# Kernel optimization log

Hardware: AMD Instinct MI355X
Metric: run time of the kernel (lower is better)

The kernel has to match this reference:

```python
import jax, jax.numpy as jnp
import numpy as np

DIM = 512
HEADS = 8
DIM_HEAD = 64
INNER = HEADS * DIM_HEAD  # 512
EPS = 1e-5


def _per_head_layernorm(t, gamma, beta):
    # t: [b, h, n, k]; gamma/beta: [h, k] (distinct LayerNorm per head)
    mu = jnp.mean(t, axis=-1, keepdims=True)
    var = jnp.mean(jnp.square(t - mu), axis=-1, keepdims=True)
    t_hat = (t - mu) * jax.lax.rsqrt(var + EPS)
    return t_hat * gamma[None, :, None, :] + beta[None, :, None, :]


def setup_inputs() -> dict:
    key = jax.random.key(0)
    ks = jax.random.split(key, 6)
    x = jax.random.normal(ks[0], (4, 8192, DIM), dtype=jnp.float32)
    # xavier_normal_ with gain=1e-4 on to_qkv weight [3*inner, dim]
    std_qkv = 1e-4 * np.sqrt(2.0 / (3 * INNER + DIM))
    W_qkv = jax.random.normal(ks[1], (3 * INNER, DIM), dtype=jnp.float32) * std_qkv
    gamma_K = jnp.ones((HEADS, DIM_HEAD), dtype=jnp.float32)
    beta_K = jnp.zeros((HEADS, DIM_HEAD), dtype=jnp.float32)
    gamma_V = jnp.ones((HEADS, DIM_HEAD), dtype=jnp.float32)
    beta_V = jnp.zeros((HEADS, DIM_HEAD), dtype=jnp.float32)
    std_out = np.sqrt(1.0 / INNER)
    W_out = jax.random.uniform(ks[2], (DIM, INNER), dtype=jnp.float32, minval=-std_out, maxval=std_out)
    b_out = jax.random.uniform(ks[3], (DIM,), dtype=jnp.float32, minval=-std_out, maxval=std_out)
    return {"x": x, "W_qkv": W_qkv, "gamma_K": gamma_K, "beta_K": beta_K,
            "gamma_V": gamma_V, "beta_V": beta_V, "W_out": W_out, "b_out": b_out}


def reference(x, W_qkv, gamma_K, beta_K, gamma_V, beta_V, W_out, b_out):
    b, n, _ = x.shape
    qkv = jnp.einsum('bnd,ed->bne', x, W_qkv)  # [b, n, 3*inner]
    q, k, v = jnp.split(qkv, 3, axis=-1)

    def to_heads(t):  # [b, n, h*k] -> [b, h, n, k]
        return t.reshape(b, n, HEADS, DIM_HEAD).transpose(0, 2, 1, 3)

    q, k, v = to_heads(q), to_heads(k), to_heads(v)
    k = _per_head_layernorm(k, gamma_K, beta_K)
    v = _per_head_layernorm(v, gamma_V, beta_V)

    # Galerkin linear attention: (K^T V)/n then Q @ (.)  -> O(n * d^2)
    p_attn = jnp.einsum('bhnk,bhnv->bhkv', k, v) / n  # [b, h, k, k]
    out = jnp.einsum('bhnk,bhkv->bhnv', q, p_attn)    # [b, h, n, k]
    out = out.transpose(0, 2, 1, 3).reshape(b, n, INNER)
    return jnp.einsum('bne,de->bnd', out, W_out) + b_out
```

## Files before the change

kernel.cpp:

```cpp
#include <hip/hip_runtime.h>


typedef __attribute__((ext_vector_type(8))) short bf16x8;
typedef __attribute__((ext_vector_type(4))) float f32x4;
typedef __attribute__((ext_vector_type(4))) unsigned short u16x4;
typedef __attribute__((ext_vector_type(4))) unsigned int u32x4;

__device__ __forceinline__ unsigned short f2bf(float f) {
  unsigned int u = __builtin_bit_cast(unsigned int, f);
  u += 0x7FFFu + ((u >> 16) & 1u);
  return (unsigned short)(u >> 16);
}

__device__ __forceinline__ unsigned int cvt2(float lo, float hi) {
  return ((unsigned int)f2bf(hi) << 16) | (unsigned int)f2bf(lo);
}

__device__ __forceinline__ f32x4 mfma16(bf16x8 a, bf16x8 b, f32x4 c) {
  return __builtin_amdgcn_mfma_f32_16x16x32_bf16(a, b, c, 0, 0, 0);
}

__device__ __forceinline__ void gload16(const void* g, void* l) {
  __builtin_amdgcn_global_load_lds(
      (const __attribute__((address_space(1))) void*)g,
      (__attribute__((address_space(3))) void*)l, 16, 0, 0);
}

__global__ void k_cvt_w(const float* __restrict__ Wqkv,
                        const float* __restrict__ Wout,
                        unsigned short* __restrict__ Wb,
                        unsigned short* __restrict__ Wob) {
  int i = blockIdx.x * 256 + threadIdx.x;
  const float4* src;
  u16x4* dst;
  if (i < 196608) { src = (const float4*)Wqkv + i; dst = (u16x4*)Wb + i; }
  else { i -= 196608; src = (const float4*)Wout + i; dst = (u16x4*)Wob + i; }
  float4 v = *src;
  u16x4 o;
  o[0] = f2bf(v.x); o[1] = f2bf(v.y); o[2] = f2bf(v.z); o[3] = f2bf(v.w);
  *dst = o;
}

__launch_bounds__(256, 3)
__global__ void k1_kvp(const float* __restrict__ x,
                       const unsigned short* __restrict__ wqkvb,
                       const float* __restrict__ gK, const float* __restrict__ bK,
                       const float* __restrict__ gV, const float* __restrict__ bV,
                       float* __restrict__ Ppart) {
  __shared__ __align__(16) unsigned short As[8192];
  __shared__ __align__(16) unsigned short Bs[8192];
  const int bid = (int)blockIdx.x;
  const int wgid = (bid & 7) * 256 + (bid >> 3);
  const int rt = wgid >> 3, h = wgid & 7;
  const int tid = (int)threadIdx.x;
  const int l = tid & 63, w = tid >> 6;
  const int wr = w >> 1, wc = w & 1;
  const int g = l >> 4, c16 = l & 15;
  const int row0 = rt * 128;
  const int swz = ((l & 7) ^ (l >> 3)) * 8;

  const float* gx = x + (size_t)(row0 + w * 32 + (l >> 3)) * 512 + swz;
  const int bcol = (w < 2) ? (512 + h * 64 + w * 32) : (1024 + h * 64 + (w - 2) * 32);
  const unsigned short* gsB = wqkvb + (bcol + (l >> 3)) * 512 + swz;
  unsigned short* la = As + w * 2048 + l * 8;

  f32x4 acc[4][4] = {};
  float4 pf[8];

#pragma unroll
  for (int j = 0; j < 4; ++j) {
    pf[2 * j]     = *(const float4*)(gx + j * 4096);
    pf[2 * j + 1] = *(const float4*)(gx + j * 4096 + 4);
  }

  for (int kt = 0; kt < 8; ++kt) {
#pragma unroll
    for (int j = 0; j < 4; ++j) {
      u32x4 c;
      c[0] = cvt2(pf[2 * j].x, pf[2 * j].y);
      c[1] = cvt2(pf[2 * j].z, pf[2 * j].w);
      c[2] = cvt2(pf[2 * j + 1].x, pf[2 * j + 1].y);
      c[3] = cvt2(pf[2 * j + 1].z, pf[2 * j + 1].w);
      *(u32x4*)(la + j * 512) = c;
    }
#pragma unroll
    for (int j = 0; j < 4; ++j)
      gload16(gsB + kt * 64 + j * 8 * 512, Bs + w * 2048 + j * 512);
    __builtin_amdgcn_sched_barrier(0);
    if (kt < 7) {
#pragma unroll
      for (int j = 0; j < 4; ++j) {
        pf[2 * j]     = *(const float4*)(gx + (kt + 1) * 64 + j * 4096);
        pf[2 * j + 1] = *(const float4*)(gx + (kt + 1) * 64 + j * 4096 + 4);
      }
      asm volatile("s_waitcnt vmcnt(8) lgkmcnt(0)" ::: "memory");
    } else {
      asm volatile("s_waitcnt vmcnt(0) lgkmcnt(0)" ::: "memory");
    }
    __builtin_amdgcn_sched_barrier(0);
    __builtin_amdgcn_s_barrier();
#pragma unroll
    for (int ks = 0; ks < 2; ++ks) {
      const int kcol = (ks * 32 + g * 8) ^ ((c16 & 7) << 3);
      bf16x8 af[4], bfv[4];
#pragma unroll
      for (int mi = 0; mi < 4; ++mi)
        af[mi] = *(const bf16x8*)&As[(wr * 64 + mi * 16 + c16) * 64 + kcol];
#pragma unroll
      for (int ni = 0; ni < 4; ++ni)
        bfv[ni] = *(const bf16x8*)&Bs[(wc * 64 + ni * 16 + c16) * 64 + kcol];
#pragma unroll
      for (int mi = 0; mi < 4; ++mi)
#pragma unroll
        for (int ni = 0; ni < 4; ++ni)
          acc[mi][ni] = mfma16(af[mi], bfv[ni], acc[mi][ni]);
    }
    __builtin_amdgcn_sched_barrier(0);
    __builtin_amdgcn_s_barrier();
  }

  const float* gamma = (wc == 0) ? gK : gV;
  const float* beta  = (wc == 0) ? bK : bV;
  float gm[4], bt[4];
#pragma unroll
  for (int ni = 0; ni < 4; ++ni) {
    gm[ni] = gamma[h * 64 + ni * 16 + c16];
    bt[ni] = beta[h * 64 + ni * 16 + c16];
  }
  unsigned short* dst = (wc == 0) ? As : Bs;
#pragma unroll
  for (int mi = 0; mi < 4; ++mi) {
    float mean4[4], rs4[4];
#pragma unroll
    for (int r = 0; r < 4; ++r) {
      float a0 = acc[mi][0][r], a1 = acc[mi][1][r];
      float a2 = acc[mi][2][r], a3 = acc[mi][3][r];
      float s1 = a0 + a1 + a2 + a3;
      float s2 = a0 * a0 + a1 * a1 + a2 * a2 + a3 * a3;
#pragma unroll
      for (int m = 1; m <= 8; m <<= 1) {
        s1 += __shfl_xor(s1, m, 64);
        s2 += __shfl_xor(s2, m, 64);
      }
      const float mean = s1 * (1.0f / 64.0f);
      const float var = s2 * (1.0f / 64.0f) - mean * mean;
      mean4[r] = mean;
      rs4[r] = rsqrtf(var + 1e-5f);
    }
    const int n0 = wr * 64 + mi * 16 + g * 4;
#pragma unroll
    for (int ni = 0; ni < 4; ++ni) {
      u16x4 o;
#pragma unroll
      for (int r = 0; r < 4; ++r)
        o[r] = f2bf((acc[mi][ni][r] - mean4[r]) * rs4[r] * gm[ni] + bt[ni]);
      *(u16x4*)&dst[(ni * 16 + c16) * 128 + (((n0 >> 3) ^ c16) << 3) + (n0 & 7)] = o;
    }
  }
  __syncthreads();

  f32x4 pacc[4] = {};
#pragma unroll
  for (int ks = 0; ks < 4; ++ks) {
    const int grp = ((ks * 4 + g) ^ c16) << 3;
    bf16x8 af = *(const bf16x8*)&As[(w * 16 + c16) * 128 + grp];
#pragma unroll
    for (int ni = 0; ni < 4; ++ni) {
      bf16x8 bv = *(const bf16x8*)&Bs[(ni * 16 + c16) * 128 + grp];
      pacc[ni] = mfma16(af, bv, pacc[ni]);
    }
  }
  const int bh = (rt >> 6) * 8 + h;
  float* Pp = Ppart + ((size_t)(bh * 64 + (rt & 63))) * 4096;
#pragma unroll
  for (int ni = 0; ni < 4; ++ni)
#pragma unroll
    for (int r = 0; r < 4; ++r)
      Pp[(w * 16 + g * 4 + r) * 64 + ni * 16 + c16] = pacc[ni][r];
}

__launch_bounds__(256)
__global__ void k_preduce(const float* __restrict__ Ppart,
                          float* __restrict__ P) {
  const int bh = blockIdx.x;
  const int e = blockIdx.y * 256 + threadIdx.x;
  const float* src = Ppart + (size_t)bh * 64 * 4096 + e;
  float s = 0.f;
#pragma unroll 8
  for (int sl = 0; sl < 64; ++sl) s += src[sl * 4096];
  P[bh * 4096 + e] = s;
}

__launch_bounds__(256)
__global__ void k3a_g(const float* __restrict__ Wqkv,
                      const float* __restrict__ P,
                      unsigned short* __restrict__ Gt) {
  __shared__ float Pl[64 * 64];
  const int bh = blockIdx.x, dd = blockIdx.y;
  const int b = bh >> 3, h = bh & 7;
  const int t = (int)threadIdx.x;
  for (int i = t; i < 1024; i += 256)
    ((float4*)Pl)[i] = ((const float4*)(P + bh * 4096))[i];
  __syncthreads();

  const int qg = t >> 6, dl = t & 63;
  const int d = dd * 64 + dl;
  float acc[16] = {};
  for (int dh = 0; dh < 64; ++dh) {
    const float wq = Wqkv[(h * 64 + dh) * 512 + d];
    const float* pr = &Pl[dh * 64 + qg * 16];
#pragma unroll
    for (int i = 0; i < 16; ++i) acc[i] += pr[i] * wq;
  }
  unsigned short* go = &Gt[(b * 512 + d) * 512 + h * 64 + qg * 16];
#pragma unroll
  for (int i = 0; i < 16; ++i) go[i] = f2bf(acc[i] * (1.0f / 8192.0f));
}

__device__ __forceinline__ void stage_tile(const unsigned short* pa,
                                           const unsigned short* pb,
                                           unsigned short* As, unsigned short* Bs,
                                           int w) {
#pragma unroll
  for (int j = 0; j < 4; ++j) {
    gload16(pa + j * 8 * 512, As + w * 2048 + j * 512);
    gload16(pb + j * 8 * 512, Bs + w * 2048 + j * 512);
  }
}

__device__ __forceinline__ void compute_tile(const unsigned short* As,
                                             const unsigned short* Bs,
                                             int wr, int wc, int g, int c16,
                                             f32x4 acc[4][4]) {
#pragma unroll
  for (int ks = 0; ks < 2; ++ks) {
    const int kcol = (ks * 32 + g * 8) ^ ((c16 & 7) << 3);
    bf16x8 af[4], bfv[4];
#pragma unroll
    for (int mi = 0; mi < 4; ++mi)
      af[mi] = *(const bf16x8*)&As[(wr * 64 + mi * 16 + c16) * 64 + kcol];
#pragma unroll
    for (int ni = 0; ni < 4; ++ni)
      bfv[ni] = *(const bf16x8*)&Bs[(wc * 64 + ni * 16 + c16) * 64 + kcol];
#pragma unroll
    for (int mi = 0; mi < 4; ++mi)
#pragma unroll
      for (int ni = 0; ni < 4; ++ni)
        acc[mi][ni] = mfma16(af[mi], bfv[ni], acc[mi][ni]);
  }
}

__launch_bounds__(256)
__global__ void k3b_m(const unsigned short* __restrict__ wob,
                      const unsigned short* __restrict__ Gt,
                      unsigned short* __restrict__ Mb) {
  __shared__ __align__(16) unsigned short As[8192];
  __shared__ __align__(16) unsigned short Bs[8192];
  const int rt = blockIdx.x, ct = blockIdx.y, b = blockIdx.z;
  const int tid = (int)threadIdx.x;
  const int l = tid & 63, w = tid >> 6;
  const int wr = w >> 1, wc = w & 1;
  const int g = l >> 4, c16 = l & 15;
  const int row0 = rt * 128, col0 = ct * 128;
  const int swz = ((l & 7) ^ (l >> 3)) * 8;

  const unsigned short* gsA = wob + (row0 + w * 32 + (l >> 3)) * 512 + swz;
  const unsigned short* gsB = Gt + b * 262144 + (col0 + w * 32 + (l >> 3)) * 512 + swz;

  f32x4 acc[4][4] = {};
  for (int kt = 0; kt < 8; ++kt) {
    stage_tile(gsA + kt * 64, gsB + kt * 64, As, Bs, w);
    __syncthreads();
    compute_tile(As, Bs, wr, wc, g, c16, acc);
    __syncthreads();
  }

#pragma unroll
  for (int mi = 0; mi < 4; ++mi)
#pragma unroll
    for (int ni = 0; ni < 4; ++ni) {
      const int colg = col0 + wc * 64 + ni * 16 + c16;
#pragma unroll
      for (int r = 0; r < 4; ++r) {
        const int rowg = row0 + wr * 64 + mi * 16 + g * 4 + r;
        Mb[(b * 512 + rowg) * 512 + colg] = f2bf(acc[mi][ni][r]);
      }
    }
}

__launch_bounds__(256, 3)
__global__ void k4_final(const float* __restrict__ x,
                         const unsigned short* __restrict__ Mb,
                         const float* __restrict__ bout,
                         float* __restrict__ y) {
  __shared__ __align__(16) unsigned short As[8192];
  __shared__ __align__(16) unsigned short Bs[8192];
  const int bid = (int)blockIdx.x;
  const int wgid = (bid & 7) * 128 + (bid >> 3);
  const int rt = wgid >> 2, ct = wgid & 3;
  const int tid = (int)threadIdx.x;
  const int l = tid & 63, w = tid >> 6;
  const int wr = w >> 1, wc = w & 1;
  const int g = l >> 4, c16 = l & 15;
  const int row0 = rt * 128, col0 = ct * 128;
  const int bb = row0 >> 13;
  const int swz = ((l & 7) ^ (l >> 3)) * 8;

  const float* gx = x + (size_t)(row0 + w * 32 + (l >> 3)) * 512 + swz;
  const unsigned short* gsB =
      Mb + (size_t)bb * 262144 + (col0 + w * 32 + (l >> 3)) * 512 + swz;
  unsigned short* la = As + w * 2048 + l * 8;

  f32x4 acc[4][4] = {};
  float4 pf[8];
#pragma unroll
  for (int j = 0; j < 4; ++j) {
    pf[2 * j]     = *(const float4*)(gx + j * 4096);
    pf[2 * j + 1] = *(const float4*)(gx + j * 4096 + 4);
  }

  for (int kt = 0; kt < 8; ++kt) {
#pragma unroll
    for (int j = 0; j < 4; ++j) {
      u32x4 c;
      c[0] = cvt2(pf[2 * j].x, pf[2 * j].y);
      c[1] = cvt2(pf[2 * j].z, pf[2 * j].w);
      c[2] = cvt2(pf[2 * j + 1].x, pf[2 * j + 1].y);
      c[3] = cvt2(pf[2 * j + 1].z, pf[2 * j + 1].w);
      *(u32x4*)(la + j * 512) = c;
    }
#pragma unroll
    for (int j = 0; j < 4; ++j)
      gload16(gsB + kt * 64 + j * 8 * 512, Bs + w * 2048 + j * 512);
    __builtin_amdgcn_sched_barrier(0);
    if (kt < 7) {
#pragma unroll
      for (int j = 0; j < 4; ++j) {
        pf[2 * j]     = *(const float4*)(gx + (kt + 1) * 64 + j * 4096);
        pf[2 * j + 1] = *(const float4*)(gx + (kt + 1) * 64 + j * 4096 + 4);
      }
      asm volatile("s_waitcnt vmcnt(8) lgkmcnt(0)" ::: "memory");
    } else {
      asm volatile("s_waitcnt vmcnt(0) lgkmcnt(0)" ::: "memory");
    }
    __builtin_amdgcn_sched_barrier(0);
    __builtin_amdgcn_s_barrier();
#pragma unroll
    for (int ks = 0; ks < 2; ++ks) {
      const int kcol = (ks * 32 + g * 8) ^ ((c16 & 7) << 3);
      bf16x8 af[4], bfv[4];
#pragma unroll
      for (int mi = 0; mi < 4; ++mi)
        af[mi] = *(const bf16x8*)&As[(wr * 64 + mi * 16 + c16) * 64 + kcol];
#pragma unroll
      for (int ni = 0; ni < 4; ++ni)
        bfv[ni] = *(const bf16x8*)&Bs[(wc * 64 + ni * 16 + c16) * 64 + kcol];
#pragma unroll
      for (int mi = 0; mi < 4; ++mi)
#pragma unroll
        for (int ni = 0; ni < 4; ++ni)
          acc[mi][ni] = mfma16(af[mi], bfv[ni], acc[mi][ni]);
    }
    __builtin_amdgcn_sched_barrier(0);
    __builtin_amdgcn_s_barrier();
  }

  float bo[4];
#pragma unroll
  for (int ni = 0; ni < 4; ++ni)
    bo[ni] = bout[col0 + wc * 64 + ni * 16 + c16];
#pragma unroll
  for (int mi = 0; mi < 4; ++mi)
#pragma unroll
    for (int ni = 0; ni < 4; ++ni) {
      const int colg = col0 + wc * 64 + ni * 16 + c16;
#pragma unroll
      for (int r = 0; r < 4; ++r) {
        const int rowg = row0 + wr * 64 + mi * 16 + g * 4 + r;
        y[rowg * 512 + colg] = acc[mi][ni][r] + bo[ni];
      }
    }
}

extern "C" void kernel_launch(void* const* d_in, const int* in_sizes, int n_in,
                              void* d_out, int out_size, void* d_ws, size_t ws_size,
                              hipStream_t stream) {
  (void)in_sizes; (void)n_in; (void)out_size; (void)ws_size;
  const float* x    = (const float*)d_in[0];
  const float* Wqkv = (const float*)d_in[1];
  const float* gK   = (const float*)d_in[2];
  const float* bK   = (const float*)d_in[3];
  const float* gV   = (const float*)d_in[4];
  const float* bV   = (const float*)d_in[5];
  const float* Wout = (const float*)d_in[6];
  const float* bout = (const float*)d_in[7];
  float* y = (float*)d_out;

  char* w = (char*)d_ws;
  unsigned short* Wb    = (unsigned short*)(w);
  unsigned short* Wob   = (unsigned short*)(w + 1572864);
  float*          P     = (float*)         (w + 2097152);
  unsigned short* Gt    = (unsigned short*)(w + 2621440);
  unsigned short* Mb    = (unsigned short*)(w + 4718592);
  float*          Ppart = (float*)         (w + 6815744);

  k_cvt_w<<<1024, 256, 0, stream>>>(Wqkv, Wout, Wb, Wob);

  k1_kvp<<<2048, 256, 0, stream>>>(x, Wb, gK, bK, gV, bV, Ppart);
  k_preduce<<<dim3(32, 16), 256, 0, stream>>>(Ppart, P);
  k3a_g<<<dim3(32, 8), 256, 0, stream>>>(Wqkv, P, Gt);
  k3b_m<<<dim3(4, 4, 4), 256, 0, stream>>>(Wob, Gt, Mb);
  k4_final<<<1024, 256, 0, stream>>>(x, Mb, bout, y);
}
```

Baseline: 127.3 us.

## Pre-convert x to bf16 and stage both GEMM operands via direct LDS loads

```diff
diff --git a/kernel.cpp b/kernel.cpp
--- a/kernel.cpp
+++ b/kernel.cpp
@@ -26,23 +26,65 @@
       (__attribute__((address_space(3))) void*)l, 16, 0, 0);
 }
 
-__global__ void k_cvt_w(const float* __restrict__ Wqkv,
-                        const float* __restrict__ Wout,
-                        unsigned short* __restrict__ Wb,
-                        unsigned short* __restrict__ Wob) {
+__global__ void k_cvt_all(const float* __restrict__ x,
+                          const float* __restrict__ Wqkv,
+                          const float* __restrict__ Wout,
+                          unsigned short* __restrict__ xb,
+                          unsigned short* __restrict__ Wb,
+                          unsigned short* __restrict__ Wob) {
   int i = blockIdx.x * 256 + threadIdx.x;
   const float4* src;
   u16x4* dst;
-  if (i < 196608) { src = (const float4*)Wqkv + i; dst = (u16x4*)Wb + i; }
-  else { i -= 196608; src = (const float4*)Wout + i; dst = (u16x4*)Wob + i; }
+  if (i < 4194304) {
+    src = (const float4*)x + i;    dst = (u16x4*)xb + i;
+  } else if (i < 4390912) {
+    i -= 4194304;
+    src = (const float4*)Wqkv + i; dst = (u16x4*)Wb + i;
+  } else {
+    i -= 4390912;
+    src = (const float4*)Wout + i; dst = (u16x4*)Wob + i;
+  }
   float4 v = *src;
   u16x4 o;
   o[0] = f2bf(v.x); o[1] = f2bf(v.y); o[2] = f2bf(v.z); o[3] = f2bf(v.w);
   *dst = o;
 }
 
-__launch_bounds__(256, 3)
-__global__ void k1_kvp(const float* __restrict__ x,
+__device__ __forceinline__ void stage_tile(const unsigned short* pa,
+                                           const unsigned short* pb,
+                                           unsigned short* As, unsigned short* Bs,
+                                           int w) {
+#pragma unroll
+  for (int j = 0; j < 4; ++j) {
+    gload16(pa + j * 8 * 512, As + w * 2048 + j * 512);
+    gload16(pb + j * 8 * 512, Bs + w * 2048 + j * 512);
+  }
+}
+
+__device__ __forceinline__ void compute_tile(const unsigned short* As,
+                                             const unsigned short* Bs,
+                                             int wr, int wc, int g, int c16,
+                                             f32x4 acc[4][4]) {
+#pragma unroll
+  for (int ks = 0; ks < 2; ++ks) {
+    const int kcol = (ks * 32 + g * 8) ^ ((c16 & 7) << 3);
+    bf16x8 af[4], bfv[4];
+#pragma unroll
+    for (int mi = 0; mi < 4; ++mi)
+      af[mi] = *(const bf16x8*)&As[(wr * 64 + mi * 16 + c16) * 64 + kcol];
+#pragma unroll
+    for (int ni = 0; ni < 4; ++ni)
+      bfv[ni] = *(const bf16x8*)&Bs[(wc * 64 + ni * 16 + c16) * 64 + kcol];
+#pragma unroll
+    for (int mi = 0; mi < 4; ++mi)
+#pragma unroll
+      for (int ni = 0; ni < 4; ++ni)
+        acc[mi][ni] = mfma16(af[mi], bfv[ni], acc[mi][ni]);
+  }
+}
+
+__launch_bounds__(256)
+__global__ void k1_kvp(const unsigned short* __restrict__ xb,
                        const unsigned short* __restrict__ wqkvb,
                        const float* __restrict__ gK, const float* __restrict__ bK,
                        const float* __restrict__ gV, const float* __restrict__ bV,
@@ -59,64 +101,16 @@
   const int row0 = rt * 128;
   const int swz = ((l & 7) ^ (l >> 3)) * 8;
 
-  const float* gx = x + (size_t)(row0 + w * 32 + (l >> 3)) * 512 + swz;
+  const unsigned short* gsA = xb + (row0 + w * 32 + (l >> 3)) * 512 + swz;
   const int bcol = (w < 2) ? (512 + h * 64 + w * 32) : (1024 + h * 64 + (w - 2) * 32);
   const unsigned short* gsB = wqkvb + (bcol + (l >> 3)) * 512 + swz;
-  unsigned short* la = As + w * 2048 + l * 8;
 
   f32x4 acc[4][4] = {};
-  float4 pf[8];
-
-#pragma unroll
-  for (int j = 0; j < 4; ++j) {
-    pf[2 * j]     = *(const float4*)(gx + j * 4096);
-    pf[2 * j + 1] = *(const float4*)(gx + j * 4096 + 4);
-  }
-
   for (int kt = 0; kt < 8; ++kt) {
-#pragma unroll
-    for (int j = 0; j < 4; ++j) {
-      u32x4 c;
-      c[0] = cvt2(pf[2 * j].x, pf[2 * j].y);
-      c[1] = cvt2(pf[2 * j].z, pf[2 * j].w);
-      c[2] = cvt2(pf[2 * j + 1].x, pf[2 * j + 1].y);
-      c[3] = cvt2(pf[2 * j + 1].z, pf[2 * j + 1].w);
-      *(u32x4*)(la + j * 512) = c;
-    }
-#pragma unroll
-    for (int j = 0; j < 4; ++j)
-      gload16(gsB + kt * 64 + j * 8 * 512, Bs + w * 2048 + j * 512);
-    __builtin_amdgcn_sched_barrier(0);
-    if (kt < 7) {
-#pragma unroll
-      for (int j = 0; j < 4; ++j) {
-        pf[2 * j]     = *(const float4*)(gx + (kt + 1) * 64 + j * 4096);
-        pf[2 * j + 1] = *(const float4*)(gx + (kt + 1) * 64 + j * 4096 + 4);
-      }
-      asm volatile("s_waitcnt vmcnt(8) lgkmcnt(0)" ::: "memory");
-    } else {
-      asm volatile("s_waitcnt vmcnt(0) lgkmcnt(0)" ::: "memory");
-    }
-    __builtin_amdgcn_sched_barrier(0);
-    __builtin_amdgcn_s_barrier();
-#pragma unroll
-    for (int ks = 0; ks < 2; ++ks) {
-      const int kcol = (ks * 32 + g * 8) ^ ((c16 & 7) << 3);
-      bf16x8 af[4], bfv[4];
-#pragma unroll
-      for (int mi = 0; mi < 4; ++mi)
-        af[mi] = *(const bf16x8*)&As[(wr * 64 + mi * 16 + c16) * 64 + kcol];
-#pragma unroll
-      for (int ni = 0; ni < 4; ++ni)
-        bfv[ni] = *(const bf16x8*)&Bs[(wc * 64 + ni * 16 + c16) * 64 + kcol];
-#pragma unroll
-      for (int mi = 0; mi < 4; ++mi)
-#pragma unroll
-        for (int ni = 0; ni < 4; ++ni)
-          acc[mi][ni] = mfma16(af[mi], bfv[ni], acc[mi][ni]);
-    }
-    __builtin_amdgcn_sched_barrier(0);
-    __builtin_amdgcn_s_barrier();
+    stage_tile(gsA + kt * 64, gsB + kt * 64, As, Bs, w);
+    __syncthreads();
+    compute_tile(As, Bs, wr, wc, g, c16, acc);
+    __syncthreads();
   }
 
   const float* gamma = (wc == 0) ? gK : gV;
@@ -127,6 +121,7 @@
     gm[ni] = gamma[h * 64 + ni * 16 + c16];
     bt[ni] = beta[h * 64 + ni * 16 + c16];
   }
+
   unsigned short* dst = (wc == 0) ? As : Bs;
 #pragma unroll
   for (int mi = 0; mi < 4; ++mi) {
@@ -215,39 +210,6 @@
   unsigned short* go = &Gt[(b * 512 + d) * 512 + h * 64 + qg * 16];
 #pragma unroll
   for (int i = 0; i < 16; ++i) go[i] = f2bf(acc[i] * (1.0f / 8192.0f));
-}
-
-__device__ __forceinline__ void stage_tile(const unsigned short* pa,
-                                           const unsigned short* pb,
-                                           unsigned short* As, unsigned short* Bs,
-                                           int w) {
-#pragma unroll
-  for (int j = 0; j < 4; ++j) {
-    gload16(pa + j * 8 * 512, As + w * 2048 + j * 512);
-    gload16(pb + j * 8 * 512, Bs + w * 2048 + j * 512);
-  }
-}
-
-__device__ __forceinline__ void compute_tile(const unsigned short* As,
-                                             const unsigned short* Bs,
-                                             int wr, int wc, int g, int c16,
-                                             f32x4 acc[4][4]) {
-#pragma unroll
-  for (int ks = 0; ks < 2; ++ks) {
-    const int kcol = (ks * 32 + g * 8) ^ ((c16 & 7) << 3);
-    bf16x8 af[4], bfv[4];
-#pragma unroll
-    for (int mi = 0; mi < 4; ++mi)
-      af[mi] = *(const bf16x8*)&As[(wr * 64 + mi * 16 + c16) * 64 + kcol];
-#pragma unroll
-    for (int ni = 0; ni < 4; ++ni)
-      bfv[ni] = *(const bf16x8*)&Bs[(wc * 64 + ni * 16 + c16) * 64 + kcol];
-#pragma unroll
-    for (int mi = 0; mi < 4; ++mi)
-#pragma unroll
-      for (int ni = 0; ni < 4; ++ni)
-        acc[mi][ni] = mfma16(af[mi], bfv[ni], acc[mi][ni]);
-  }
 }
 
 __launch_bounds__(256)
@@ -397,16 +359,17 @@
   float* y = (float*)d_out;
 
   char* w = (char*)d_ws;
-  unsigned short* Wb    = (unsigned short*)(w);
-  unsigned short* Wob   = (unsigned short*)(w + 1572864);
-  float*          P     = (float*)         (w + 2097152);
-  unsigned short* Gt    = (unsigned short*)(w + 2621440);
-  unsigned short* Mb    = (unsigned short*)(w + 4718592);
-  float*          Ppart = (float*)         (w + 6815744);
-
-  k_cvt_w<<<1024, 256, 0, stream>>>(Wqkv, Wout, Wb, Wob);
-
-  k1_kvp<<<2048, 256, 0, stream>>>(x, Wb, gK, bK, gV, bV, Ppart);
+  unsigned short* xb    = (unsigned short*)(w);
+  unsigned short* Wb    = (unsigned short*)(w + 33554432);
+  unsigned short* Wob   = (unsigned short*)(w + 35127296);
+  float*          P     = (float*)         (w + 35651584);
+  unsigned short* Gt    = (unsigned short*)(w + 36175872);
+  unsigned short* Mb    = (unsigned short*)(w + 38273024);
+  float*          Ppart = (float*)         (w + 40370176);
+
+  k_cvt_all<<<17408, 256, 0, stream>>>(x, Wqkv, Wout, xb, Wb, Wob);
+
+  k1_kvp<<<2048, 256, 0, stream>>>(xb, Wb, gK, bK, gV, bV, Ppart);
   k_preduce<<<dim3(32, 16), 256, 0, stream>>>(Ppart, P);
   k3a_g<<<dim3(32, 8), 256, 0, stream>>>(Wqkv, P, Gt);
   k3b_m<<<dim3(4, 4, 4), 256, 0, stream>>>(Wob, Gt, Mb);
```

Result: slower. 134.2 us (+5.4%).

## Double-buffer x prefetch in k1 and fuse partial-P reduction into k3a

Applied to the files above, without the earlier changes.

```diff
diff --git a/kernel.cpp b/kernel.cpp
--- a/kernel.cpp
+++ b/kernel.cpp
@@ -65,59 +65,100 @@
   unsigned short* la = As + w * 2048 + l * 8;
 
   f32x4 acc[4][4] = {};
-  float4 pf[8];
-
-#pragma unroll
-  for (int j = 0; j < 4; ++j) {
-    pf[2 * j]     = *(const float4*)(gx + j * 4096);
-    pf[2 * j + 1] = *(const float4*)(gx + j * 4096 + 4);
-  }
-
-  for (int kt = 0; kt < 8; ++kt) {
-#pragma unroll
-    for (int j = 0; j < 4; ++j) {
-      u32x4 c;
-      c[0] = cvt2(pf[2 * j].x, pf[2 * j].y);
-      c[1] = cvt2(pf[2 * j].z, pf[2 * j].w);
-      c[2] = cvt2(pf[2 * j + 1].x, pf[2 * j + 1].y);
-      c[3] = cvt2(pf[2 * j + 1].z, pf[2 * j + 1].w);
-      *(u32x4*)(la + j * 512) = c;
-    }
-#pragma unroll
-    for (int j = 0; j < 4; ++j)
-      gload16(gsB + kt * 64 + j * 8 * 512, Bs + w * 2048 + j * 512);
-    __builtin_amdgcn_sched_barrier(0);
-    if (kt < 7) {
-#pragma unroll
-      for (int j = 0; j < 4; ++j) {
-        pf[2 * j]     = *(const float4*)(gx + (kt + 1) * 64 + j * 4096);
-        pf[2 * j + 1] = *(const float4*)(gx + (kt + 1) * 64 + j * 4096 + 4);
-      }
-      asm volatile("s_waitcnt vmcnt(8) lgkmcnt(0)" ::: "memory");
-    } else {
-      asm volatile("s_waitcnt vmcnt(0) lgkmcnt(0)" ::: "memory");
-    }
-    __builtin_amdgcn_sched_barrier(0);
-    __builtin_amdgcn_s_barrier();
-#pragma unroll
-    for (int ks = 0; ks < 2; ++ks) {
-      const int kcol = (ks * 32 + g * 8) ^ ((c16 & 7) << 3);
-      bf16x8 af[4], bfv[4];
-#pragma unroll
-      for (int mi = 0; mi < 4; ++mi)
-        af[mi] = *(const bf16x8*)&As[(wr * 64 + mi * 16 + c16) * 64 + kcol];
-#pragma unroll
-      for (int ni = 0; ni < 4; ++ni)
-        bfv[ni] = *(const bf16x8*)&Bs[(wc * 64 + ni * 16 + c16) * 64 + kcol];
-#pragma unroll
-      for (int mi = 0; mi < 4; ++mi)
-#pragma unroll
-        for (int ni = 0; ni < 4; ++ni)
-          acc[mi][ni] = mfma16(af[mi], bfv[ni], acc[mi][ni]);
-    }
-    __builtin_amdgcn_sched_barrier(0);
-    __builtin_amdgcn_s_barrier();
-  }
+  float4 pA[8], pB[8];
+
+#define LOAD_PF(PF, T)                                                  \
+  {                                                                     \
+    _Pragma("unroll")                                                   \
+    for (int j = 0; j < 4; ++j) {                                       \
+      PF[2 * j]     = *(const float4*)(gx + (T) * 64 + j * 4096);       \
+      PF[2 * j + 1] = *(const float4*)(gx + (T) * 64 + j * 4096 + 4);   \
+    }                                                                   \
+  }
+#define CVT_WRITE(PF)                                                   \
+  {                                                                     \
+    _Pragma("unroll")                                                   \
+    for (int j = 0; j < 4; ++j) {                                       \
+      u32x4 c;                                                          \
+      c[0] = cvt2(PF[2 * j].x, PF[2 * j].y);                            \
+      c[1] = cvt2(PF[2 * j].z, PF[2 * j].w);                            \
+      c[2] = cvt2(PF[2 * j + 1].x, PF[2 * j + 1].y);                    \
+      c[3] = cvt2(PF[2 * j + 1].z, PF[2 * j + 1].w);                    \
+      *(u32x4*)(la + j * 512) = c;                                      \
+    }                                                                   \
+  }
+#define STAGE_B(T)                                                      \
+  {                                                                     \
+    _Pragma("unroll")                                                   \
+    for (int j = 0; j < 4; ++j)                                         \
+      gload16(gsB + (T) * 64 + j * 8 * 512, Bs + w * 2048 + j * 512);   \
+  }
+#define COMPUTE()                                                       \
+  {                                                                     \
+    _Pragma("unroll")                                                   \
+    for (int ks = 0; ks < 2; ++ks) {                                    \
+      const int kcol = (ks * 32 + g * 8) ^ ((c16 & 7) << 3);            \
+      bf16x8 af[4], bfv[4];                                             \
+      _Pragma("unroll")                                                 \
+      for (int mi = 0; mi < 4; ++mi)                                    \
+        af[mi] = *(const bf16x8*)&As[(wr * 64 + mi * 16 + c16) * 64 + kcol]; \
+      _Pragma("unroll")                                                 \
+      for (int ni = 0; ni < 4; ++ni)                                    \
+        bfv[ni] = *(const bf16x8*)&Bs[(wc * 64 + ni * 16 + c16) * 64 + kcol]; \
+      _Pragma("unroll")                                                 \
+      for (int mi = 0; mi < 4; ++mi)                                    \
+        _Pragma("unroll")                                               \
+        for (int ni = 0; ni < 4; ++ni)                                  \
+          acc[mi][ni] = mfma16(af[mi], bfv[ni], acc[mi][ni]);           \
+    }                                                                   \
+  }
+
+  LOAD_PF(pA, 0);
+  LOAD_PF(pB, 1);
+
+#pragma unroll
+  for (int p = 0; p < 4; ++p) {
+    {
+      const int t = 2 * p;
+      STAGE_B(t);
+      CVT_WRITE(pA);
+      __builtin_amdgcn_sched_barrier(0);
+      if (p < 3) {
+        LOAD_PF(pA, t + 2);
+        __builtin_amdgcn_sched_barrier(0);
+        asm volatile("s_waitcnt vmcnt(8) lgkmcnt(0)" ::: "memory");
+      } else {
+        asm volatile("s_waitcnt vmcnt(0) lgkmcnt(0)" ::: "memory");
+      }
+      __builtin_amdgcn_sched_barrier(0);
+      __builtin_amdgcn_s_barrier();
+      COMPUTE();
+      __builtin_amdgcn_sched_barrier(0);
+      __builtin_amdgcn_s_barrier();
+    }
+    {
+      const int t = 2 * p + 1;
+      STAGE_B(t);
+      CVT_WRITE(pB);
+      __builtin_amdgcn_sched_barrier(0);
+      if (p < 3) {
+        LOAD_PF(pB, t + 2);
+        __builtin_amdgcn_sched_barrier(0);
+        asm volatile("s_waitcnt vmcnt(8) lgkmcnt(0)" ::: "memory");
+      } else {
+        asm volatile("s_waitcnt vmcnt(0) lgkmcnt(0)" ::: "memory");
+      }
+      __builtin_amdgcn_sched_barrier(0);
+      __builtin_amdgcn_s_barrier();
+      COMPUTE();
+      __builtin_amdgcn_sched_barrier(0);
+      __builtin_amdgcn_s_barrier();
+    }
+  }
+#undef LOAD_PF
+#undef CVT_WRITE
+#undef STAGE_B
+#undef COMPUTE
 
   const float* gamma = (wc == 0) ? gK : gV;
   const float* beta  = (wc == 0) ? bK : bV;
@@ -180,41 +221,44 @@
 }
 
 __launch_bounds__(256)
-__global__ void k_preduce(const float* __restrict__ Ppart,
-                          float* __restrict__ P) {
+__global__ void k3a_g(const float* __restrict__ Wqkv,
+                      const float* __restrict__ Ppart,
+                      unsigned short* __restrict__ Gt) {
+  __shared__ float Pl[4096];
   const int bh = blockIdx.x;
-  const int e = blockIdx.y * 256 + threadIdx.x;
-  const float* src = Ppart + (size_t)bh * 64 * 4096 + e;
-  float s = 0.f;
-#pragma unroll 8
-  for (int sl = 0; sl < 64; ++sl) s += src[sl * 4096];
-  P[bh * 4096 + e] = s;
-}
-
-__launch_bounds__(256)
-__global__ void k3a_g(const float* __restrict__ Wqkv,
-                      const float* __restrict__ P,
-                      unsigned short* __restrict__ Gt) {
-  __shared__ float Pl[64 * 64];
-  const int bh = blockIdx.x, dd = blockIdx.y;
   const int b = bh >> 3, h = bh & 7;
   const int t = (int)threadIdx.x;
-  for (int i = t; i < 1024; i += 256)
-    ((float4*)Pl)[i] = ((const float4*)(P + bh * 4096))[i];
+
+  float4 a0 = {0, 0, 0, 0}, a1 = a0, a2 = a0, a3 = a0;
+  const float* base = Ppart + (size_t)bh * 262144;
+  for (int sl = 0; sl < 64; ++sl) {
+    const float4* p = (const float4*)(base + sl * 4096);
+    float4 v0 = p[t], v1 = p[t + 256], v2 = p[t + 512], v3 = p[t + 768];
+    a0.x += v0.x; a0.y += v0.y; a0.z += v0.z; a0.w += v0.w;
+    a1.x += v1.x; a1.y += v1.y; a1.z += v1.z; a1.w += v1.w;
+    a2.x += v2.x; a2.y += v2.y; a2.z += v2.z; a2.w += v2.w;
+    a3.x += v3.x; a3.y += v3.y; a3.z += v3.z; a3.w += v3.w;
+  }
+  ((float4*)Pl)[t] = a0;
+  ((float4*)Pl)[t + 256] = a1;
+  ((float4*)Pl)[t + 512] = a2;
+  ((float4*)Pl)[t + 768] = a3;
   __syncthreads();
 
   const int qg = t >> 6, dl = t & 63;
-  const int d = dd * 64 + dl;
-  float acc[16] = {};
-  for (int dh = 0; dh < 64; ++dh) {
-    const float wq = Wqkv[(h * 64 + dh) * 512 + d];
-    const float* pr = &Pl[dh * 64 + qg * 16];
-#pragma unroll
-    for (int i = 0; i < 16; ++i) acc[i] += pr[i] * wq;
-  }
-  unsigned short* go = &Gt[(b * 512 + d) * 512 + h * 64 + qg * 16];
-#pragma unroll
-  for (int i = 0; i < 16; ++i) go[i] = f2bf(acc[i] * (1.0f / 8192.0f));
+  for (int dd = 0; dd < 8; ++dd) {
+    const int d = dd * 64 + dl;
+    float acc[16] = {};
+    for (int dh = 0; dh < 64; ++dh) {
+      const float wq = Wqkv[(h * 64 + dh) * 512 + d];
+      const float* pr = &Pl[dh * 64 + qg * 16];
+#pragma unroll
+      for (int i = 0; i < 16; ++i) acc[i] += pr[i] * wq;
+    }
+    unsigned short* go = &Gt[(b * 512 + d) * 512 + h * 64 + qg * 16];
+#pragma unroll
+    for (int i = 0; i < 16; ++i) go[i] = f2bf(acc[i] * (1.0f / 8192.0f));
+  }
 }
 
 __device__ __forceinline__ void stage_tile(const unsigned short* pa,
@@ -399,16 +443,14 @@
   char* w = (char*)d_ws;
   unsigned short* Wb    = (unsigned short*)(w);
   unsigned short* Wob   = (unsigned short*)(w + 1572864);
-  float*          P     = (float*)         (w + 2097152);
-  unsigned short* Gt    = (unsigned short*)(w + 2621440);
-  unsigned short* Mb    = (unsigned short*)(w + 4718592);
-  float*          Ppart = (float*)         (w + 6815744);
+  unsigned short* Gt    = (unsigned short*)(w + 2097152);
+  unsigned short* Mb    = (unsigned short*)(w + 4194304);
+  float*          Ppart = (float*)         (w + 6291456);
 
   k_cvt_w<<<1024, 256, 0, stream>>>(Wqkv, Wout, Wb, Wob);
 
   k1_kvp<<<2048, 256, 0, stream>>>(x, Wb, gK, bK, gV, bV, Ppart);
-  k_preduce<<<dim3(32, 16), 256, 0, stream>>>(Ppart, P);
-  k3a_g<<<dim3(32, 8), 256, 0, stream>>>(Wqkv, P, Gt);
+  k3a_g<<<32, 256, 0, stream>>>(Wqkv, Ppart, Gt);
   k3b_m<<<dim3(4, 4, 4), 256, 0, stream>>>(Wob, Gt, Mb);
   k4_final<<<1024, 256, 0, stream>>>(x, Mb, bout, y);
 }
```

Result: slower. 196.3 us (median of 2 runs) (+54.2%).
